# Performance work log

Hardware: AMD Instinct MI355X
Metric: run time of the kernel (lower is better)

## Reference

```python
import jax, jax.numpy as jnp
import numpy as np
from jax import lax

B, C, H, W, NH = 16, 512, 32, 32, 8
HC = C // NH  # head channels = 64


def setup_inputs() -> dict:
    key = jax.random.key(0)
    ks = jax.random.split(key, 8)
    rn = lambda i, shape, scale: jax.random.normal(ks[i], shape, jnp.float32) * scale
    return dict(
        image=jax.random.normal(ks[0], (B, C, H, W), jnp.float32),
        watermark=jax.random.normal(ks[1], (B, C, H, W), jnp.float32),
        img_ln_w=jnp.ones((C, H, W), jnp.float32),
        img_ln_b=jnp.zeros((C, H, W), jnp.float32),
        wm_ln_w=jnp.ones((C, H, W), jnp.float32),
        wm_ln_b=jnp.zeros((C, H, W), jnp.float32),
        img_pw_w=rn(2, (3 * C, C), 0.02),
        img_pw_b=jnp.zeros((3 * C,), jnp.float32),
        img_dw_w=rn(3, (3 * C, 3, 3, 3), 0.1),
        img_dw_b=jnp.zeros((3 * C,), jnp.float32),
        wm_pw_w=rn(4, (3 * C, C), 0.02),
        wm_pw_b=jnp.zeros((3 * C,), jnp.float32),
        wm_dw_w=rn(5, (3 * C, 3, 3, 3), 0.1),
        wm_dw_b=jnp.zeros((3 * C,), jnp.float32),
        proj=rn(6, (2 * C, C), 0.02),
    )


def _layernorm(x, w, b, eps=1e-5):
    # LayerNorm over [C,H,W] per sample, elementwise affine of shape [C,H,W]
    mu = jnp.mean(x, axis=(1, 2, 3), keepdims=True)
    var = jnp.mean((x - mu) ** 2, axis=(1, 2, 3), keepdims=True)
    return (x - mu) * lax.rsqrt(var + eps) * w + b


def _dconv_proj(x, pw_w, pw_b, dw_w, dw_b):
    # pointwise 1x1 conv C -> 3C
    x = jnp.einsum('bchw,oc->bohw', x, pw_w) + pw_b[None, :, None, None]
    # depthwise 3x3 conv on 3C channels with groups=C (3 channels per group)
    x = lax.conv_general_dilated(
        x, dw_w, window_strides=(1, 1), padding='SAME',
        dimension_numbers=('NCHW', 'OIHW', 'NCHW'), feature_group_count=C)
    x = x + dw_b[None, :, None, None]
    return jnp.split(x, 3, axis=1)  # Q, K, V each [B,C,H,W]


def reference(image, watermark, img_ln_w, img_ln_b, wm_ln_w, wm_ln_b,
              img_pw_w, img_pw_b, img_dw_w, img_dw_b,
              wm_pw_w, wm_pw_b, wm_dw_w, wm_dw_b, proj):
    img = _layernorm(image, img_ln_w, img_ln_b)
    wm = _layernorm(watermark, wm_ln_w, wm_ln_b)
    Qi, Ki, Vi = _dconv_proj(img, img_pw_w, img_pw_b, img_dw_w, img_dw_b)
    Qw, Kw, Vw = _dconv_proj(wm, wm_pw_w, wm_pw_b, wm_dw_w, wm_dw_b)
    r = lambda t: t.reshape(B, NH, HC, H * W)
    Qi, Ki, Vi, Qw, Kw, Vw = map(r, (Qi, Ki, Vi, Qw, Kw, Vw))
    # NOTE: original code calls F.normalize but discards the result -> no-op.
    Kc = jnp.concatenate([Ki, Kw], axis=2)  # [B,NH,2*HC,HW]
    Vc = jnp.concatenate([Vi, Vw], axis=2)  # [B,NH,2*HC,HW]
    # scores: K_concat @ Q^T over the HW axis -> [B,NH,2*HC,HC], softmax over HC
    Ai = jax.nn.softmax(jnp.einsum('bnkp,bnqp->bnkq', Kc, Qi), axis=-1)
    Aw = jax.nn.softmax(jnp.einsum('bnkp,bnqp->bnkq', Kc, Qw), axis=-1)
    # A^T @ V_concat -> [B,NH,HC,HW]
    img_attn = jnp.einsum('bnkq,bnkp->bnqp', Ai, Vc)
    wm_attn = jnp.einsum('bnkq,bnkp->bnqp', Aw, Vc)
    attn = jnp.concatenate([img_attn, wm_attn], axis=2).reshape(B, 2 * C, H, W)
    # final channel-mixing projection: [B,H,W,2C] @ [2C,C] -> [B,C,H,W]
    return jnp.einsum('bdhw,dc->bchw', attn, proj)
```

## Files before the change

### kernel.cpp

```cpp
#include <hip/hip_runtime.h>
#include <hip/hip_bf16.h>
#include <stdint.h>

#define Bn  16
#define Cch 512
#define C3  1536
#define HWp 1024

typedef __attribute__((ext_vector_type(8))) short bf16x8;
typedef __attribute__((ext_vector_type(4))) float f32x4;

#define DEV static __device__ __forceinline__

DEV float bflo(unsigned u) { return __builtin_bit_cast(float, u << 16); }
DEV float bfhi(unsigned u) { return __builtin_bit_cast(float, u & 0xffff0000u); }
DEV unsigned short f2bf(float f) {
  __hip_bfloat16 h = __float2bfloat16(f);
  return __builtin_bit_cast(unsigned short, h);
}

DEV void async16(__hip_bfloat16* lds, const __hip_bfloat16* g) {
  __builtin_amdgcn_global_load_lds(
      (const __attribute__((address_space(1))) unsigned*)g,
      (__attribute__((address_space(3))) unsigned*)lds, 16, 0, 0);
}

__global__ __launch_bounds__(256) void k_prep(
    const float* __restrict__ img_pw_w, const float* __restrict__ wm_pw_w,
    const float* __restrict__ proj,
    __hip_bfloat16* __restrict__ Wpw, __hip_bfloat16* __restrict__ projT)
{
  int i = blockIdx.x * 256 + threadIdx.x;
  const int NW = C3 * Cch;
  if (i < NW)          Wpw[i] = __float2bfloat16(img_pw_w[i]);
  else if (i < 2 * NW) Wpw[i] = __float2bfloat16(wm_pw_w[i - NW]);
  else {
    int j = i - 2 * NW;
    int c = j >> 10, d = j & 1023;
    projT[(size_t)c * 1024 + d] = __float2bfloat16(proj[(size_t)d * 512 + c]);
  }
}

__global__ __launch_bounds__(256) void k_ln_partial(
    const float* __restrict__ image, const float* __restrict__ watermark,
    float* __restrict__ part)
{
  int blk = blockIdx.x;
  int chunk = blk & 63, b = (blk >> 6) & 15, t = blk >> 10;
  const float* x = (t ? watermark : image) + (size_t)b * Cch * HWp + chunk * 8192;
  const float4* xv = (const float4*)x;
  float s = 0.f, ss = 0.f;
#pragma unroll
  for (int i = 0; i < 8; i++) {
    float4 v = xv[threadIdx.x + i * 256];
    s  += v.x + v.y + v.z + v.w;
    ss += v.x * v.x + v.y * v.y + v.z * v.z + v.w * v.w;
  }
#pragma unroll
  for (int off = 32; off; off >>= 1) { s += __shfl_down(s, off); ss += __shfl_down(ss, off); }
  __shared__ float ls[4], lss[4];
  int wv = threadIdx.x >> 6;
  if ((threadIdx.x & 63) == 0) { ls[wv] = s; lss[wv] = ss; }
  __syncthreads();
  if (threadIdx.x == 0) {
    part[blk * 2]     = ls[0] + ls[1] + ls[2] + ls[3];
    part[blk * 2 + 1] = lss[0] + lss[1] + lss[2] + lss[3];
  }
}

__global__ void k_ln_final(const float* __restrict__ part, float* __restrict__ stats)
{
  int i = threadIdx.x;
  if (i < 32) {
    float S = 0.f, SS = 0.f;
    for (int c2 = 0; c2 < 64; c2++) { S += part[(i * 64 + c2) * 2]; SS += part[(i * 64 + c2) * 2 + 1]; }
    const float inv = 1.f / (float)(Cch * HWp);
    float mu  = S * inv;
    float var = SS * inv - mu * mu;
    stats[i]      = mu;
    stats[32 + i] = rsqrtf(var + 1e-5f);
  }
}

__global__ __launch_bounds__(256) void k_norm_t(
    const float* __restrict__ image, const float* __restrict__ watermark,
    const float* __restrict__ img_w, const float* __restrict__ img_b,
    const float* __restrict__ wm_w,  const float* __restrict__ wm_b,
    const float* __restrict__ stats, __hip_bfloat16* __restrict__ xnT)
{
  int blk = blockIdx.x;
  int ct = blk & 15, pt = (blk >> 4) & 15, b = (blk >> 8) & 15, t = blk >> 12;
  int c0 = ct * 32, p0 = pt * 64;
  const float* x   = (t ? watermark : image) + (size_t)b * Cch * HWp;
  const float* wgt = t ? wm_w : img_w;
  const float* bia = t ? wm_b : img_b;
  float mu = stats[t * 16 + b], rstd = stats[32 + t * 16 + b];
  __shared__ float tile[32 * 66];
  int tid = threadIdx.x;
  {
    int c = tid >> 3, s = tid & 7;
    const float* xr = x   + (size_t)(c0 + c) * HWp + p0;
    const float* wr = wgt + (size_t)(c0 + c) * HWp + p0;
    const float* br = bia + (size_t)(c0 + c) * HWp + p0;
#pragma unroll
    for (int j = 0; j < 2; j++) {
      int f = s + j * 8;
      float4 xv = *(const float4*)&xr[f * 4];
      float4 wv = *(const float4*)&wr[f * 4];
      float4 bv = *(const float4*)&br[f * 4];
      float n0 = (xv.x - mu) * rstd * wv.x + bv.x;
      float n1 = (xv.y - mu) * rstd * wv.y + bv.y;
      float n2 = (xv.z - mu) * rstd * wv.z + bv.z;
      float n3 = (xv.w - mu) * rstd * wv.w + bv.w;
      *(float2*)&tile[c * 66 + f * 4]     = make_float2(n0, n1);
      *(float2*)&tile[c * 66 + f * 4 + 2] = make_float2(n2, n3);
    }
  }
  __syncthreads();
  {
    int p = tid >> 2, cq = tid & 3;
    union { unsigned short us[8]; uint4 v4; } pk;
#pragma unroll
    for (int j = 0; j < 8; j++) pk.us[j] = f2bf(tile[(cq * 8 + j) * 66 + p]);
    __hip_bfloat16* dst = xnT + ((size_t)(t * 16 + b)) * HWp * Cch
                        + (size_t)(p0 + p) * Cch + c0 + cq * 8;
    *(uint4*)dst = pk.v4;
  }
}

template<int MI, int Kdim, int Ncols, bool OBF, bool HB>
DEV void gemm_core(const __hip_bfloat16* __restrict__ A,
                   const __hip_bfloat16* __restrict__ Bt,
                   const float* __restrict__ bias, void* __restrict__ Cout)
{
  constexpr int MT = MI * 32;
  __shared__ __hip_bfloat16 As[MT * 64];
  __shared__ __hip_bfloat16 Bs[128 * 64];
  const int tid = threadIdx.x, lane = tid & 63, wv = tid >> 6;
  const int lr = lane & 15, lq = lane >> 4;
  const int wm = (wv >> 1) * (MI * 16), wn = (wv & 1) * 64;
  const int m0 = blockIdx.y * MT, n0 = blockIdx.x * 128;
  f32x4 acc[MI][4] = {};
  const int srow = tid >> 3, sseg = (tid & 7) * 8;
  for (int k0 = 0; k0 < Kdim; k0 += 64) {
#pragma unroll
    for (int c = 0; c < MI; c++) {
      int row = srow + c * 32;
      async16(&As[row * 64 + sseg], &A[(size_t)(m0 + row) * Kdim + k0 + sseg]);
    }
#pragma unroll
    for (int c = 0; c < 4; c++) {
      int row = srow + c * 32;
      async16(&Bs[row * 64 + sseg], &Bt[(size_t)(n0 + row) * Kdim + k0 + sseg]);
    }
    __syncthreads();
#pragma unroll
    for (int ks = 0; ks < 2; ks++) {
      bf16x8 af[MI], bfr[4];
#pragma unroll
      for (int mi = 0; mi < MI; mi++)
        af[mi]  = *(const bf16x8*)&As[(wm + mi * 16 + lr) * 64 + ks * 32 + lq * 8];
#pragma unroll
      for (int ni = 0; ni < 4; ni++)
        bfr[ni] = *(const bf16x8*)&Bs[(wn + ni * 16 + lr) * 64 + ks * 32 + lq * 8];
#pragma unroll
      for (int mi = 0; mi < MI; mi++)
#pragma unroll
        for (int ni = 0; ni < 4; ni++)
          acc[mi][ni] = __builtin_amdgcn_mfma_f32_16x16x32_bf16(af[mi], bfr[ni], acc[mi][ni], 0, 0, 0);
    }
    __syncthreads();
  }
#pragma unroll
  for (int mi = 0; mi < MI; mi++) {
    int mrow = m0 + wm + mi * 16 + lq * 4;
#pragma unroll
    for (int ni = 0; ni < 4; ni++) {
      int ncol = n0 + wn + ni * 16 + lr;
#pragma unroll
      for (int r = 0; r < 4; r++) {
        float y = acc[mi][ni][r];
        int row = mrow + r;
        if (HB) y += bias[row];
        if (OBF) ((__hip_bfloat16*)Cout)[(size_t)row * Ncols + ncol] = __float2bfloat16(y);
        else     ((float*)Cout)[(size_t)row * Ncols + ncol] = y;
      }
    }
  }
}

__global__ __launch_bounds__(256) void k_pw_gemm(
    const __hip_bfloat16* __restrict__ Wpw, const __hip_bfloat16* __restrict__ xnT,
    const float* __restrict__ img_pw_b, const float* __restrict__ wm_pw_b,
    __hip_bfloat16* __restrict__ Y)
{
  int bz = blockIdx.z, t = bz >> 4;
  gemm_core<4, 512, 1024, true, true>(
      Wpw + (size_t)t * C3 * Cch,
      xnT + (size_t)bz * HWp * Cch,
      t ? wm_pw_b : img_pw_b,
      Y + (size_t)bz * C3 * HWp);
}

__global__ __launch_bounds__(256) void k_proj_gemm(
    const __hip_bfloat16* __restrict__ projT, const __hip_bfloat16* __restrict__ attnT,
    float* __restrict__ out)
{
  int b = blockIdx.z;
  gemm_core<2, 1024, 1024, false, false>(
      projT, attnT + (size_t)b * HWp * 1024, nullptr, out + (size_t)b * Cch * HWp);
}

__global__ __launch_bounds__(256) void k_dw(
    const __hip_bfloat16* __restrict__ Y,
    const float* __restrict__ img_dw_w, const float* __restrict__ img_dw_b,
    const float* __restrict__ wm_dw_w,  const float* __restrict__ wm_dw_b,
    __hip_bfloat16* __restrict__ QKV)
{
  int idx = blockIdx.x * 256 + threadIdx.x;
  int w0 = (idx & 3) * 8;
  int h  = (idx >> 2) & 31;
  int g  = __builtin_amdgcn_readfirstlane((idx >> 7) & 511);
  int tb = __builtin_amdgcn_readfirstlane(idx >> 16);
  int t  = tb >> 4;
  const float* dww = (t ? wm_dw_w : img_dw_w) + g * 81;
  const float* dwb = (t ? wm_dw_b : img_dw_b) + g * 3;
  const __hip_bfloat16* base = Y + ((size_t)tb * C3 + g * 3) * HWp;
  float acc[3][8];
#pragma unroll
  for (int o = 0; o < 3; o++) {
    float bv = dwb[o];
#pragma unroll
    for (int w = 0; w < 8; w++) acc[o][w] = bv;
  }
  const bool mlo = (w0 == 0), mhi = (w0 == 24);
#pragma unroll
  for (int i = 0; i < 3; i++) {
#pragma unroll
    for (int kh = 0; kh < 3; kh++) {
      int hh = h + kh - 1;
      if ((unsigned)hh > 31u) continue;
      const unsigned* up = (const unsigned*)(base + i * HWp + hh * 32 + (w0 - 2));
      float v[12];
#pragma unroll
      for (int d2 = 0; d2 < 6; d2++) { unsigned u = up[d2]; v[d2*2] = bflo(u); v[d2*2+1] = bfhi(u); }
      if (mlo) { v[0] = 0.f; v[1] = 0.f; }
      if (mhi) { v[10] = 0.f; v[11] = 0.f; }
#pragma unroll
      for (int o = 0; o < 3; o++) {
        float wk0 = dww[o*27 + i*9 + kh*3 + 0];
        float wk1 = dww[o*27 + i*9 + kh*3 + 1];
        float wk2 = dww[o*27 + i*9 + kh*3 + 2];
#pragma unroll
        for (int w = 0; w < 8; w++)
          acc[o][w] += v[w + 1] * wk0 + v[w + 2] * wk1 + v[w + 3] * wk2;
      }
    }
  }
#pragma unroll
  for (int o = 0; o < 3; o++) {
    union { unsigned short us[8]; uint4 v4; } pk;
#pragma unroll
    for (int w = 0; w < 8; w++) pk.us[w] = f2bf(acc[o][w]);
    *(uint4*)(QKV + ((size_t)tb * C3 + g * 3 + o) * HWp + h * 32 + w0) = pk.v4;
  }
}

__global__ __launch_bounds__(256) void k_attn_scores(
    const __hip_bfloat16* __restrict__ QKV, __hip_bfloat16* __restrict__ ATg)
{
  int blk = blockIdx.x, m = blk & 1, bn = blk >> 1;
  int b = bn >> 3, nh = bn & 7;
  int tid = threadIdx.x, lane = tid & 63, wv = tid >> 6;
  int lr = lane & 15, lq = lane >> 4;
  const __hip_bfloat16* kbase[2];
#pragma unroll
  for (int kt = 0; kt < 2; kt++) {
    int krow = wv * 32 + kt * 16 + lr;
    int tk = krow >> 6, hc = krow & 63;
    kbase[kt] = QKV + (((size_t)(tk * 16 + b)) * C3 + 512 + nh * 64 + hc) * HWp + lq * 8;
  }
  const __hip_bfloat16* qbase[4];
#pragma unroll
  for (int qt = 0; qt < 4; qt++)
    qbase[qt] = QKV + (((size_t)(m * 16 + b)) * C3 + nh * 64 + qt * 16 + lr) * HWp + lq * 8;

  f32x4 acc[2][4] = {};
  for (int p0 = 0; p0 < HWp; p0 += 32) {
    bf16x8 af[2];
#pragma unroll
    for (int kt = 0; kt < 2; kt++) af[kt] = *(const bf16x8*)(kbase[kt] + p0);
#pragma unroll
    for (int qt = 0; qt < 4; qt++) {
      bf16x8 bq = *(const bf16x8*)(qbase[qt] + p0);
#pragma unroll
      for (int kt = 0; kt < 2; kt++)
        acc[kt][qt] = __builtin_amdgcn_mfma_f32_16x16x32_bf16(af[kt], bq, acc[kt][qt], 0, 0, 0);
    }
  }
  __shared__ float S[64][129];
  __shared__ float red[2][2][128];
#pragma unroll
  for (int kt = 0; kt < 2; kt++)
#pragma unroll
    for (int qt = 0; qt < 4; qt++)
#pragma unroll
      for (int r = 0; r < 4; r++)
        S[qt * 16 + lr][wv * 32 + kt * 16 + lq * 4 + r] = acc[kt][qt][r];
  __syncthreads();
  int k = tid & 127, qh = tid >> 7;
  float vals[32], mx = -1e30f;
#pragma unroll
  for (int j = 0; j < 32; j++) { vals[j] = S[qh * 32 + j][k]; mx = fmaxf(mx, vals[j]); }
  red[0][qh][k] = mx;
  __syncthreads();
  float M = fmaxf(red[0][0][k], red[0][1][k]);
  float ssum = 0.f;
#pragma unroll
  for (int j = 0; j < 32; j++) { vals[j] = __expf(vals[j] - M); ssum += vals[j]; }
  red[1][qh][k] = ssum;
  __syncthreads();
  float inv = 1.f / (red[1][0][k] + red[1][1][k]);
  __hip_bfloat16* outp = ATg + (((size_t)(bn * 2 + m)) * 64 + qh * 32) * 128 + k;
#pragma unroll
  for (int j = 0; j < 32; j++) outp[(size_t)j * 128] = __float2bfloat16(vals[j] * inv);
}

__global__ __launch_bounds__(256) void k_attn_out(
    const __hip_bfloat16* __restrict__ QKV, const __hip_bfloat16* __restrict__ ATg,
    __hip_bfloat16* __restrict__ attnT)
{
  int blk = blockIdx.x, pc = blk & 3, bn = blk >> 2, b = bn >> 3, nh = bn & 7;
  int tid = threadIdx.x, lane = tid & 63, wv = tid >> 6;
  int lr = lane & 15, lq = lane >> 4;
  __shared__ __hip_bfloat16 ATs[64][136];
  __shared__ __hip_bfloat16 VTs[64][136];
  for (int m = 0; m < 2; m++) {
    __syncthreads();
    {
      const __hip_bfloat16* src = ATg + ((size_t)(bn * 2 + m)) * 64 * 128;
#pragma unroll
      for (int s = 0; s < 4; s++) {
        int id = tid + s * 256, row = id >> 4, seg = (id & 15) * 8;
        *(uint4*)&ATs[row][seg] = *(const uint4*)&src[row * 128 + seg];
      }
    }
    for (int ps = 0; ps < 4; ps++) {
      int p0 = pc * 256 + ps * 64;
      __syncthreads();
#pragma unroll
      for (int s = 0; s < 4; s++) {
        int id = tid + s * 256;
        int k = id >> 3, seg = (id & 7) * 8;
        int tk = k >> 6, hc = k & 63;
        const __hip_bfloat16* vp =
            QKV + (((size_t)(tk * 16 + b)) * C3 + 1024 + nh * 64 + hc) * HWp + p0 + seg;
        uint4 pkv = *(const uint4*)vp;
        unsigned short* pv = (unsigned short*)&pkv;
#pragma unroll
        for (int e = 0; e < 8; e++) *(unsigned short*)&VTs[seg + e][k] = pv[e];
      }
      __syncthreads();
      f32x4 oacc[4] = {};
#pragma unroll
      for (int ks = 0; ks < 4; ks++) {
        bf16x8 bv = *(const bf16x8*)&VTs[wv * 16 + lr][ks * 32 + lq * 8];
#pragma unroll
        for (int qt = 0; qt < 4; qt++) {
          bf16x8 av = *(const bf16x8*)&ATs[qt * 16 + lr][ks * 32 + lq * 8];
          oacc[qt] = __builtin_amdgcn_mfma_f32_16x16x32_bf16(av, bv, oacc[qt], 0, 0, 0);
        }
      }
#pragma unroll
      for (int qt = 0; qt < 4; qt++) {
        int q = qt * 16 + lq * 4;
        int d = nh * 128 + m * 64 + q;
        int p = p0 + wv * 16 + lr;
        union { unsigned short us[4]; uint2 v2; } pk;
#pragma unroll
        for (int r = 0; r < 4; r++) pk.us[r] = f2bf(oacc[qt][r]);
        *(uint2*)&attnT[((size_t)b * HWp + p) * 1024 + d] = pk.v2;
      }
    }
  }
}

extern "C" void kernel_launch(void* const* d_in, const int* in_sizes, int n_in,
                              void* d_out, int out_size, void* d_ws, size_t ws_size,
                              hipStream_t stream)
{
  (void)in_sizes; (void)n_in; (void)out_size; (void)ws_size;
  const float* image     = (const float*)d_in[0];
  const float* watermark = (const float*)d_in[1];
  const float* img_ln_w  = (const float*)d_in[2];
  const float* img_ln_b  = (const float*)d_in[3];
  const float* wm_ln_w   = (const float*)d_in[4];
  const float* wm_ln_b   = (const float*)d_in[5];
  const float* img_pw_w  = (const float*)d_in[6];
  const float* img_pw_b  = (const float*)d_in[7];
  const float* img_dw_w  = (const float*)d_in[8];
  const float* img_dw_b  = (const float*)d_in[9];
  const float* wm_pw_w   = (const float*)d_in[10];
  const float* wm_pw_b   = (const float*)d_in[11];
  const float* wm_dw_w   = (const float*)d_in[12];
  const float* wm_dw_b   = (const float*)d_in[13];
  const float* proj      = (const float*)d_in[14];

  char* ws = (char*)d_ws;
  __hip_bfloat16* Wpw    = (__hip_bfloat16*)(ws + 0);
  __hip_bfloat16* projT  = (__hip_bfloat16*)(ws + 3145728);
  float*          lnpart = (float*)(ws + 4194304);
  float*          stats  = (float*)(ws + 4210688);
  __hip_bfloat16* xnT    = (__hip_bfloat16*)(ws + 5242880);
  __hip_bfloat16* attnT  = xnT;
  __hip_bfloat16* Y      = (__hip_bfloat16*)(ws + 41943040);
  __hip_bfloat16* ATg    = Y;
  __hip_bfloat16* QKV    = (__hip_bfloat16*)(ws + 142606336);

  k_prep<<<8192, 256, 0, stream>>>(img_pw_w, wm_pw_w, proj, Wpw, projT);
  k_ln_partial<<<2048, 256, 0, stream>>>(image, watermark, lnpart);
  k_ln_final<<<1, 64, 0, stream>>>(lnpart, stats);
  k_norm_t<<<8192, 256, 0, stream>>>(image, watermark, img_ln_w, img_ln_b,
                                     wm_ln_w, wm_ln_b, stats, xnT);
  dim3 gpw(8, 12, 32);
  k_pw_gemm<<<gpw, 256, 0, stream>>>(Wpw, xnT, img_pw_b, wm_pw_b, Y);
  k_dw<<<8192, 256, 0, stream>>>(Y, img_dw_w, img_dw_b, wm_dw_w, wm_dw_b, QKV);
  k_attn_scores<<<256, 256, 0, stream>>>(QKV, ATg);
  k_attn_out<<<512, 256, 0, stream>>>(QKV, ATg, attnT);
  dim3 gpj(8, 8, 16);
  k_proj_gemm<<<gpj, 256, 0, stream>>>(projT, attnT, (float*)d_out);
}
```

Baseline: 392.5 us.

## Split attention scores over key halves and reuse V tiles across both queries

k_attn_scores now splits the 128 key rows into two blocks (512 blocks instead of 256), so each wave handles one 16-row K tile. Softmax runs over 64 columns per block, and results are staged in LDS for coalesced 16-byte stores. k_attn_out loads both attention matrices up front and loads each V tile once for both m, cutting V global reads and barriers by half. V transposition now packs four k rows into 8-byte LDS writes instead of scalar 2-byte stores. The cost is more LDS per block in k_attn_out.

```diff
diff --git a/kernel.cpp b/kernel.cpp
--- a/kernel.cpp
+++ b/kernel.cpp
@@ -269,61 +269,58 @@
 __global__ __launch_bounds__(256) void k_attn_scores(
     const __hip_bfloat16* __restrict__ QKV, __hip_bfloat16* __restrict__ ATg)
 {
-  int blk = blockIdx.x, m = blk & 1, bn = blk >> 1;
+  int blk = blockIdx.x, kh = blk & 1, m = (blk >> 1) & 1, bn = blk >> 2;
   int b = bn >> 3, nh = bn & 7;
   int tid = threadIdx.x, lane = tid & 63, wv = tid >> 6;
   int lr = lane & 15, lq = lane >> 4;
-  const __hip_bfloat16* kbase[2];
-#pragma unroll
-  for (int kt = 0; kt < 2; kt++) {
-    int krow = wv * 32 + kt * 16 + lr;
-    int tk = krow >> 6, hc = krow & 63;
-    kbase[kt] = QKV + (((size_t)(tk * 16 + b)) * C3 + 512 + nh * 64 + hc) * HWp + lq * 8;
-  }
+  const __hip_bfloat16* kb =
+      QKV + (((size_t)(kh * 16 + b)) * C3 + 512 + nh * 64 + (wv * 16 + lr)) * HWp + lq * 8;
   const __hip_bfloat16* qbase[4];
 #pragma unroll
   for (int qt = 0; qt < 4; qt++)
     qbase[qt] = QKV + (((size_t)(m * 16 + b)) * C3 + nh * 64 + qt * 16 + lr) * HWp + lq * 8;
 
-  f32x4 acc[2][4] = {};
+  f32x4 acc[4] = {};
   for (int p0 = 0; p0 < HWp; p0 += 32) {
-    bf16x8 af[2];
-#pragma unroll
-    for (int kt = 0; kt < 2; kt++) af[kt] = *(const bf16x8*)(kbase[kt] + p0);
+    bf16x8 bk = *(const bf16x8*)(kb + p0);
 #pragma unroll
     for (int qt = 0; qt < 4; qt++) {
-      bf16x8 bq = *(const bf16x8*)(qbase[qt] + p0);
-#pragma unroll
-      for (int kt = 0; kt < 2; kt++)
-        acc[kt][qt] = __builtin_amdgcn_mfma_f32_16x16x32_bf16(af[kt], bq, acc[kt][qt], 0, 0, 0);
-    }
-  }
-  __shared__ float S[64][129];
-  __shared__ float red[2][2][128];
-#pragma unroll
-  for (int kt = 0; kt < 2; kt++)
-#pragma unroll
-    for (int qt = 0; qt < 4; qt++)
-#pragma unroll
-      for (int r = 0; r < 4; r++)
-        S[qt * 16 + lr][wv * 32 + kt * 16 + lq * 4 + r] = acc[kt][qt][r];
-  __syncthreads();
-  int k = tid & 127, qh = tid >> 7;
-  float vals[32], mx = -1e30f;
-#pragma unroll
-  for (int j = 0; j < 32; j++) { vals[j] = S[qh * 32 + j][k]; mx = fmaxf(mx, vals[j]); }
-  red[0][qh][k] = mx;
-  __syncthreads();
-  float M = fmaxf(red[0][0][k], red[0][1][k]);
+      bf16x8 aq = *(const bf16x8*)(qbase[qt] + p0);
+      acc[qt] = __builtin_amdgcn_mfma_f32_16x16x32_bf16(aq, bk, acc[qt], 0, 0, 0);
+    }
+  }
+  __shared__ float S[64][65];
+  __shared__ float redmax[4][64];
+  __shared__ float redsum[4][64];
+  __shared__ __hip_bfloat16 Ash[64][72];
+#pragma unroll
+  for (int qt = 0; qt < 4; qt++)
+#pragma unroll
+    for (int r = 0; r < 4; r++)
+      S[qt * 16 + lq * 4 + r][wv * 16 + lr] = acc[qt][r];
+  __syncthreads();
+  int k = tid & 63, sub = tid >> 6;
+  float vals[16], mx = -1e30f;
+#pragma unroll
+  for (int j = 0; j < 16; j++) { vals[j] = S[sub * 16 + j][k]; mx = fmaxf(mx, vals[j]); }
+  redmax[sub][k] = mx;
+  __syncthreads();
+  float M = fmaxf(fmaxf(redmax[0][k], redmax[1][k]), fmaxf(redmax[2][k], redmax[3][k]));
   float ssum = 0.f;
 #pragma unroll
-  for (int j = 0; j < 32; j++) { vals[j] = __expf(vals[j] - M); ssum += vals[j]; }
-  red[1][qh][k] = ssum;
-  __syncthreads();
-  float inv = 1.f / (red[1][0][k] + red[1][1][k]);
-  __hip_bfloat16* outp = ATg + (((size_t)(bn * 2 + m)) * 64 + qh * 32) * 128 + k;
-#pragma unroll
-  for (int j = 0; j < 32; j++) outp[(size_t)j * 128] = __float2bfloat16(vals[j] * inv);
+  for (int j = 0; j < 16; j++) { vals[j] = __expf(vals[j] - M); ssum += vals[j]; }
+  redsum[sub][k] = ssum;
+  __syncthreads();
+  float inv = 1.f / (redsum[0][k] + redsum[1][k] + redsum[2][k] + redsum[3][k]);
+#pragma unroll
+  for (int j = 0; j < 16; j++) Ash[sub * 16 + j][k] = __float2bfloat16(vals[j] * inv);
+  __syncthreads();
+  __hip_bfloat16* outp = ATg + ((size_t)(bn * 2 + m)) * 64 * 128 + kh * 64;
+#pragma unroll
+  for (int s = 0; s < 2; s++) {
+    int id = tid + s * 256, row = id >> 3, seg = (id & 7) * 8;
+    *(uint4*)&outp[(size_t)row * 128 + seg] = *(const uint4*)&Ash[row][seg];
+  }
 }
 
 __global__ __launch_bounds__(256) void k_attn_out(
@@ -333,41 +330,45 @@
   int blk = blockIdx.x, pc = blk & 3, bn = blk >> 2, b = bn >> 3, nh = bn & 7;
   int tid = threadIdx.x, lane = tid & 63, wv = tid >> 6;
   int lr = lane & 15, lq = lane >> 4;
-  __shared__ __hip_bfloat16 ATs[64][136];
+  __shared__ __hip_bfloat16 ATs[2][64][136];
   __shared__ __hip_bfloat16 VTs[64][136];
+#pragma unroll
   for (int m = 0; m < 2; m++) {
+    const __hip_bfloat16* src = ATg + ((size_t)(bn * 2 + m)) * 64 * 128;
+#pragma unroll
+    for (int s = 0; s < 4; s++) {
+      int id = tid + s * 256, row = id >> 4, seg = (id & 15) * 8;
+      *(uint4*)&ATs[m][row][seg] = *(const uint4*)&src[row * 128 + seg];
+    }
+  }
+  const int vk0 = (tid >> 3) * 4, vps = (tid & 7) * 8;
+  for (int ps = 0; ps < 4; ps++) {
+    int p0 = pc * 256 + ps * 64;
     __syncthreads();
-    {
-      const __hip_bfloat16* src = ATg + ((size_t)(bn * 2 + m)) * 64 * 128;
-#pragma unroll
-      for (int s = 0; s < 4; s++) {
-        int id = tid + s * 256, row = id >> 4, seg = (id & 15) * 8;
-        *(uint4*)&ATs[row][seg] = *(const uint4*)&src[row * 128 + seg];
-      }
-    }
-    for (int ps = 0; ps < 4; ps++) {
-      int p0 = pc * 256 + ps * 64;
-      __syncthreads();
-#pragma unroll
-      for (int s = 0; s < 4; s++) {
-        int id = tid + s * 256;
-        int k = id >> 3, seg = (id & 7) * 8;
-        int tk = k >> 6, hc = k & 63;
-        const __hip_bfloat16* vp =
-            QKV + (((size_t)(tk * 16 + b)) * C3 + 1024 + nh * 64 + hc) * HWp + p0 + seg;
-        uint4 pkv = *(const uint4*)vp;
-        unsigned short* pv = (unsigned short*)&pkv;
-#pragma unroll
-        for (int e = 0; e < 8; e++) *(unsigned short*)&VTs[seg + e][k] = pv[e];
-      }
-      __syncthreads();
+    union { uint4 v4; unsigned short us[8]; } ld[4];
+#pragma unroll
+    for (int j = 0; j < 4; j++) {
+      int kk = vk0 + j, tk = kk >> 6, hc = kk & 63;
+      ld[j].v4 = *(const uint4*)(QKV +
+          (((size_t)(tk * 16 + b)) * C3 + 1024 + nh * 64 + hc) * HWp + p0 + vps);
+    }
+#pragma unroll
+    for (int e = 0; e < 8; e++) {
+      uint2 w;
+      w.x = (unsigned)ld[0].us[e] | ((unsigned)ld[1].us[e] << 16);
+      w.y = (unsigned)ld[2].us[e] | ((unsigned)ld[3].us[e] << 16);
+      *(uint2*)&VTs[vps + e][vk0] = w;
+    }
+    __syncthreads();
+#pragma unroll
+    for (int m = 0; m < 2; m++) {
       f32x4 oacc[4] = {};
 #pragma unroll
       for (int ks = 0; ks < 4; ks++) {
         bf16x8 bv = *(const bf16x8*)&VTs[wv * 16 + lr][ks * 32 + lq * 8];
 #pragma unroll
         for (int qt = 0; qt < 4; qt++) {
-          bf16x8 av = *(const bf16x8*)&ATs[qt * 16 + lr][ks * 32 + lq * 8];
+          bf16x8 av = *(const bf16x8*)&ATs[m][qt * 16 + lr][ks * 32 + lq * 8];
           oacc[qt] = __builtin_amdgcn_mfma_f32_16x16x32_bf16(av, bv, oacc[qt], 0, 0, 0);
         }
       }
@@ -425,7 +426,7 @@
   dim3 gpw(8, 12, 32);
   k_pw_gemm<<<gpw, 256, 0, stream>>>(Wpw, xnT, img_pw_b, wm_pw_b, Y);
   k_dw<<<8192, 256, 0, stream>>>(Y, img_dw_w, img_dw_b, wm_dw_w, wm_dw_b, QKV);
-  k_attn_scores<<<256, 256, 0, stream>>>(QKV, ATg);
+  k_attn_scores<<<512, 256, 0, stream>>>(QKV, ATg);
   k_attn_out<<<512, 256, 0, stream>>>(QKV, ATg, attnT);
   dim3 gpj(8, 8, 16);
   k_proj_gemm<<<gpj, 256, 0, stream>>>(projT, attnT, (float*)d_out);
```

After: 393.4 us. No clear change (+0.2%).
